# Kernel optimization log

Hardware: AMD Instinct MI355X
Metric: run time of the kernel (lower is better)

## Reference

```python
import jax, jax.numpy as jnp
import numpy as np

NUM_HEADS = 16


def setup_inputs() -> dict:
    key = jax.random.key(0)
    kq, kk, kv = jax.random.split(key, 3)
    b, s, h = 1, 4096, 1024
    q = jax.random.normal(kq, (b, s, h), dtype=jnp.float32)
    k = jax.random.normal(kk, (b, s, h), dtype=jnp.float32)
    v = jax.random.normal(kv, (b, s, h), dtype=jnp.float32)
    return {"q": q, "k": k, "v": v}


def reference(q, k, v):
    b, s, hd = q.shape
    n = NUM_HEADS
    d = hd // n
    # b s (n d) -> b s n d
    qh = q.reshape(b, s, n, d)
    kh = k.reshape(b, s, n, d)
    vh = v.reshape(b, s, n, d)
    scale = 1.0 / jnp.sqrt(jnp.float32(d))
    # non-causal flash-attention math: softmax(qk^T * scale) v
    scores = jnp.einsum('bqnd,bknd->bnqk', qh, kh) * scale  # [b, n, s, s]
    probs = jax.nn.softmax(scores, axis=-1)
    out = jnp.einsum('bnqk,bknd->bqnd', probs, vh)  # [b, s, n, d]
    return out.reshape(b, s, hd)
```

## Files before the change

kernel.cpp:

```cpp
#include <hip/hip_runtime.h>

#define S_   4096
#define H_   1024
#define NH_  16
#define NT_  64
#define SCALE_LOG2E 0.18033688011112042f

typedef __attribute__((ext_vector_type(8)))  short short8;
typedef __attribute__((ext_vector_type(16))) float f32x16;

__device__ __forceinline__ unsigned short f2bf(float x) {
    union { float f; unsigned u; } c; c.f = x;
    unsigned r = c.u + 0x7fffu + ((c.u >> 16) & 1u);
    return (unsigned short)(r >> 16);
}
__device__ __forceinline__ unsigned pk2(float a, float b) {
    return (unsigned)f2bf(a) | ((unsigned)f2bf(b) << 16);
}
__device__ __forceinline__ unsigned pkt(float a, float b) {
    union { float f; unsigned u; } ca, cb; ca.f = a; cb.f = b;
    return __builtin_amdgcn_perm(cb.u, ca.u, 0x07060302u);
}

__global__ __launch_bounds__(256) void prepack(
    const float* __restrict__ k, const float* __restrict__ v,
    unsigned short* __restrict__ kp, unsigned short* __restrict__ vtp)
{
    const int t  = threadIdx.x;
    const int kt = blockIdx.x, hd = blockIdx.y;
    const size_t tb = ((size_t)hd * NT_ + kt) * 4096;
    uint4* gk = (uint4*)(kp + tb);
    uint4* gv = (uint4*)(vtp + tb);

    #pragma unroll
    for (int it = 0; it < 2; ++it) {
        int idx = t + 256 * it;
        {
            int key = idx >> 3, kc = idx & 7;
            const float* src = k + (size_t)(kt * 64 + key) * H_ + hd * 64 + kc * 8;
            float4 a = *(const float4*)src;
            float4 b = *(const float4*)(src + 4);
            uint4 w;
            w.x = pk2(a.x, a.y); w.y = pk2(a.z, a.w);
            w.z = pk2(b.x, b.y); w.w = pk2(b.z, b.w);
            gk[kc * 64 + key] = w;
        }
        {
            int d = idx & 63, kc = idx >> 6;
            const float* src = v + (size_t)(kt * 64 + kc * 8) * H_ + hd * 64 + d;
            float p[8];
            #pragma unroll
            for (int j = 0; j < 8; ++j) p[j] = src[(size_t)j * H_];
            uint4 w;
            w.x = pk2(p[0], p[1]); w.y = pk2(p[2], p[3]);
            w.z = pk2(p[4], p[5]); w.w = pk2(p[6], p[7]);
            gv[idx] = w;
        }
    }
}

__global__ __launch_bounds__(256, 3) void attn_main(
    const float* __restrict__ q,
    const unsigned short* __restrict__ kp,
    const unsigned short* __restrict__ vtp,
    float* __restrict__ out)
{
    __shared__ __align__(16) float sO[2 * 2048];
    __shared__ float sL[2 * 64];

    const int t   = threadIdx.x;
    const int b   = blockIdx.x;
    const int xcd = b & 7;
    const int bi  = b >> 3;
    const int hd  = xcd * 2 + (bi >> 6);
    const int qt  = bi & 63;

    const int w    = t >> 6;
    const int lane = t & 63;
    const int l31  = lane & 31;
    const int lhi  = lane >> 5;
    const int qh   = w >> 1;
    const int kh   = w & 1;

    const unsigned short* gK = kp  + (size_t)hd * NT_ * 4096;
    const unsigned short* gV = vtp + (size_t)hd * NT_ * 4096;

    short8 qf[4];
    {
        const float* qb = q + (size_t)(qt * 64 + qh * 32 + l31) * H_ + hd * 64 + lhi * 8;
        #pragma unroll
        for (int c = 0; c < 4; ++c) {
            float4 a  = *(const float4*)(qb + c * 16);
            float4 bb = *(const float4*)(qb + c * 16 + 4);
            union { short8 v; unsigned u[4]; } f;
            f.u[0] = pk2(a.x * SCALE_LOG2E, a.y * SCALE_LOG2E);
            f.u[1] = pk2(a.z * SCALE_LOG2E, a.w * SCALE_LOG2E);
            f.u[2] = pk2(bb.x * SCALE_LOG2E, bb.y * SCALE_LOG2E);
            f.u[3] = pk2(bb.z * SCALE_LOG2E, bb.w * SCALE_LOG2E);
            qf[c] = f.v;
        }
    }

    f32x16 Oacc[2];
    #pragma unroll
    for (int h = 0; h < 2; ++h)
        #pragma unroll
        for (int r = 0; r < 16; ++r) Oacc[h][r] = 0.0f;
    float2 ls2; ls2.x = 0.0f; ls2.y = 0.0f;

    const int kOff = (kh * 32 + l31) * 8 + lhi * 512;
    const int vOff = l31 * 8 + (kh * 4 + lhi) * 512;
    const unsigned short* pK = gK + kOff;
    const unsigned short* pV = gV + vOff;

    short8 kfA[4], vfA[4], kfB[4], vfB[4];

#define LOADF(KF, VF, tile)                                                  \
    {                                                                        \
        const unsigned short* kt_ = pK + (size_t)(tile) * 4096;              \
        const unsigned short* vt_ = pV + (size_t)(tile) * 4096;              \
        KF[0] = *(const short8*)(kt_);                                       \
        KF[1] = *(const short8*)(kt_ + 1024);                                \
        KF[2] = *(const short8*)(kt_ + 2048);                                \
        KF[3] = *(const short8*)(kt_ + 3072);                                \
        VF[0] = *(const short8*)(vt_);                                       \
        VF[1] = *(const short8*)(vt_ + 256);                                 \
        VF[2] = *(const short8*)(vt_ + 1024);                                \
        VF[3] = *(const short8*)(vt_ + 1280);                                \
    }

#define COMPUTE(KF, VF)                                                      \
    {                                                                        \
        f32x16 st;                                                           \
        _Pragma("unroll")                                                    \
        for (int r_ = 0; r_ < 16; ++r_) st[r_] = 0.0f;                       \
        st = __builtin_amdgcn_mfma_f32_32x32x16_bf16(KF[0], qf[0], st, 0, 0, 0); \
        st = __builtin_amdgcn_mfma_f32_32x32x16_bf16(KF[1], qf[1], st, 0, 0, 0); \
        st = __builtin_amdgcn_mfma_f32_32x32x16_bf16(KF[2], qf[2], st, 0, 0, 0); \
        st = __builtin_amdgcn_mfma_f32_32x32x16_bf16(KF[3], qf[3], st, 0, 0, 0); \
        unsigned pu[8];                                                      \
        _Pragma("unroll")                                                    \
        for (int i2_ = 0; i2_ < 8; ++i2_) {                                  \
            float p0 = __builtin_amdgcn_exp2f(st[2 * i2_]);                  \
            float p1 = __builtin_amdgcn_exp2f(st[2 * i2_ + 1]);              \
            ls2.x += p0; ls2.y += p1;                                        \
            pu[i2_] = pkt(p0, p1);                                           \
        }                                                                    \
        _Pragma("unroll")                                                    \
        for (int c_ = 0; c_ < 2; ++c_) {                                     \
            unsigned a0 = pu[4 * c_],     b0 = pu[4 * c_ + 2];               \
            unsigned a1 = pu[4 * c_ + 1], b1 = pu[4 * c_ + 3];               \
                                   \
            asm("v_permlane32_swap_b32 %0, %1" : "+v"(a0), "+v"(b0));        \
            asm("v_permlane32_swap_b32 %0, %1" : "+v"(a1), "+v"(b1));        \
            union { short8 v; unsigned u[4]; } pf;                           \
            pf.u[0] = a0; pf.u[1] = a1; pf.u[2] = b0; pf.u[3] = b1;          \
            Oacc[0] = __builtin_amdgcn_mfma_f32_32x32x16_bf16(pf.v, VF[2 * c_],     Oacc[0], 0, 0, 0); \
            Oacc[1] = __builtin_amdgcn_mfma_f32_32x32x16_bf16(pf.v, VF[2 * c_ + 1], Oacc[1], 0, 0, 0); \
        }                                                                    \
    }

    LOADF(kfA, vfA, 0);
    for (int kt2 = 0; kt2 < 31; ++kt2) {
        LOADF(kfB, vfB, 2 * kt2 + 1);
        COMPUTE(kfA, vfA);
        LOADF(kfA, vfA, 2 * kt2 + 2);
        COMPUTE(kfB, vfB);
    }
    LOADF(kfB, vfB, 63);
    COMPUTE(kfA, vfA);
    COMPUTE(kfB, vfB);

#undef LOADF
#undef COMPUTE

    float lsum = ls2.x + ls2.y;
    lsum += __shfl_xor(lsum, 32);
    if (lhi == 0) sL[kh * 64 + qh * 32 + l31] = lsum;
    if (kh == 1) {
        float* o = sO + qh * 2048;
        #pragma unroll
        for (int h = 0; h < 2; ++h)
            #pragma unroll
            for (int r = 0; r < 16; ++r)
                o[h * 1024 + r * 64 + lane] = Oacc[h][r];
    }
    __syncthreads();
    if (kh == 0) {
        float linv[4][4];
        #pragma unroll
        for (int qd = 0; qd < 4; ++qd) {
            int base = qh * 32 + 8 * qd + 4 * lhi;
            float4 a  = *(const float4*)(sL + base);
            float4 bb = *(const float4*)(sL + 64 + base);
            linv[qd][0] = __builtin_amdgcn_rcpf(a.x + bb.x);
            linv[qd][1] = __builtin_amdgcn_rcpf(a.y + bb.y);
            linv[qd][2] = __builtin_amdgcn_rcpf(a.z + bb.z);
            linv[qd][3] = __builtin_amdgcn_rcpf(a.w + bb.w);
        }
        const float* o = sO + qh * 2048;
        #pragma unroll
        for (int h = 0; h < 2; ++h)
            #pragma unroll
            for (int qd = 0; qd < 4; ++qd)
                #pragma unroll
                for (int e = 0; e < 4; ++e) {
                    int r   = 4 * qd + e;
                    int row = qh * 32 + e + 8 * qd + 4 * lhi;
                    float val = (Oacc[h][r] + o[h * 1024 + r * 64 + lane]) * linv[qd][e];
                    out[(size_t)(qt * 64 + row) * H_ + hd * 64 + h * 32 + l31] = val;
                }
    }
}

extern "C" void kernel_launch(void* const* d_in, const int* in_sizes, int n_in,
                              void* d_out, int out_size, void* d_ws, size_t ws_size,
                              hipStream_t stream) {
    const float* q = (const float*)d_in[0];
    const float* k = (const float*)d_in[1];
    const float* v = (const float*)d_in[2];
    float* out = (float*)d_out;

    unsigned short* kp  = (unsigned short*)d_ws;
    unsigned short* vtp = kp + (size_t)NH_ * NT_ * 4096;

    prepack<<<dim3(NT_, NH_), 256, 0, stream>>>(k, v, kp, vtp);
    attn_main<<<dim3(1024), 256, 0, stream>>>(q, kp, vtp, out);
}
```

Before: 178.6 us.

## Double query tile per block to reuse K/V fragments across two query subtiles

Each warp now handles two 32-row query subtiles instead of one, so every K/V fragment loaded from global memory feeds twice as many MFMAs. The grid is halved to 512 blocks of 128 queries, and occupancy drops to 2 blocks per CU to make room for the larger accumulator register set. s_setprio hints are placed around the MFMA groups so this wave gets priority while the other waves run exp and permute work. The change cuts K/V load traffic per FLOP, at the cost of higher register pressure, fewer resident waves and only 512 blocks to spread across the CUs.

```diff
diff --git a/kernel.cpp b/kernel.cpp
--- a/kernel.cpp
+++ b/kernel.cpp
@@ -59,35 +59,36 @@
     }
 }
 
-__global__ __launch_bounds__(256, 3) void attn_main(
+__global__ __launch_bounds__(256, 2) void attn_main(
     const float* __restrict__ q,
     const unsigned short* __restrict__ kp,
     const unsigned short* __restrict__ vtp,
     float* __restrict__ out)
 {
-    __shared__ __align__(16) float sO[2 * 2048];
-    __shared__ float sL[2 * 64];
+    __shared__ __align__(16) float sO[4 * 2048];
+    __shared__ float sL[2 * 128];
 
     const int t   = threadIdx.x;
     const int b   = blockIdx.x;
     const int xcd = b & 7;
     const int bi  = b >> 3;
-    const int hd  = xcd * 2 + (bi >> 6);
-    const int qt  = bi & 63;
+    const int hd  = xcd * 2 + (bi >> 5);
+    const int qt  = bi & 31;
 
     const int w    = t >> 6;
     const int lane = t & 63;
     const int l31  = lane & 31;
     const int lhi  = lane >> 5;
-    const int qh   = w >> 1;
+    const int qg   = w >> 1;
     const int kh   = w & 1;
 
     const unsigned short* gK = kp  + (size_t)hd * NT_ * 4096;
     const unsigned short* gV = vtp + (size_t)hd * NT_ * 4096;
 
-    short8 qf[4];
-    {
-        const float* qb = q + (size_t)(qt * 64 + qh * 32 + l31) * H_ + hd * 64 + lhi * 8;
+    short8 qf[2][4];
+    #pragma unroll
+    for (int s = 0; s < 2; ++s) {
+        const float* qb = q + (size_t)(qt * 128 + qg * 64 + s * 32 + l31) * H_ + hd * 64 + lhi * 8;
         #pragma unroll
         for (int c = 0; c < 4; ++c) {
             float4 a  = *(const float4*)(qb + c * 16);
@@ -97,16 +98,23 @@
             f.u[1] = pk2(a.z * SCALE_LOG2E, a.w * SCALE_LOG2E);
             f.u[2] = pk2(bb.x * SCALE_LOG2E, bb.y * SCALE_LOG2E);
             f.u[3] = pk2(bb.z * SCALE_LOG2E, bb.w * SCALE_LOG2E);
-            qf[c] = f.v;
-        }
-    }
-
-    f32x16 Oacc[2];
-    #pragma unroll
-    for (int h = 0; h < 2; ++h)
-        #pragma unroll
-        for (int r = 0; r < 16; ++r) Oacc[h][r] = 0.0f;
-    float2 ls2; ls2.x = 0.0f; ls2.y = 0.0f;
+            qf[s][c] = f.v;
+        }
+    }
+
+    f32x16 Oacc[2][2];
+    #pragma unroll
+    for (int s = 0; s < 2; ++s)
+        #pragma unroll
+        for (int h = 0; h < 2; ++h)
+            #pragma unroll
+            for (int r = 0; r < 16; ++r) Oacc[s][h][r] = 0.0f;
+    float2 ls[2];
+    ls[0].x = 0.0f; ls[0].y = 0.0f; ls[1].x = 0.0f; ls[1].y = 0.0f;
+
+    f32x16 zero16;
+    #pragma unroll
+    for (int r = 0; r < 16; ++r) zero16[r] = 0.0f;
 
     const int kOff = (kh * 32 + l31) * 8 + lhi * 512;
     const int vOff = l31 * 8 + (kh * 4 + lhi) * 512;
@@ -131,32 +139,36 @@
 
 #define COMPUTE(KF, VF)                                                      \
     {                                                                        \
-        f32x16 st;                                                           \
         _Pragma("unroll")                                                    \
-        for (int r_ = 0; r_ < 16; ++r_) st[r_] = 0.0f;                       \
-        st = __builtin_amdgcn_mfma_f32_32x32x16_bf16(KF[0], qf[0], st, 0, 0, 0); \
-        st = __builtin_amdgcn_mfma_f32_32x32x16_bf16(KF[1], qf[1], st, 0, 0, 0); \
-        st = __builtin_amdgcn_mfma_f32_32x32x16_bf16(KF[2], qf[2], st, 0, 0, 0); \
-        st = __builtin_amdgcn_mfma_f32_32x32x16_bf16(KF[3], qf[3], st, 0, 0, 0); \
-        unsigned pu[8];                                                      \
-        _Pragma("unroll")                                                    \
-        for (int i2_ = 0; i2_ < 8; ++i2_) {                                  \
-            float p0 = __builtin_amdgcn_exp2f(st[2 * i2_]);                  \
-            float p1 = __builtin_amdgcn_exp2f(st[2 * i2_ + 1]);              \
-            ls2.x += p0; ls2.y += p1;                                        \
-            pu[i2_] = pkt(p0, p1);                                           \
-        }                                                                    \
-        _Pragma("unroll")                                                    \
-        for (int c_ = 0; c_ < 2; ++c_) {                                     \
-            unsigned a0 = pu[4 * c_],     b0 = pu[4 * c_ + 2];               \
-            unsigned a1 = pu[4 * c_ + 1], b1 = pu[4 * c_ + 3];               \
+        for (int s_ = 0; s_ < 2; ++s_) {                                     \
+            __builtin_amdgcn_s_setprio(1);                                   \
+            f32x16 st = __builtin_amdgcn_mfma_f32_32x32x16_bf16(KF[0], qf[s_][0], zero16, 0, 0, 0); \
+            st = __builtin_amdgcn_mfma_f32_32x32x16_bf16(KF[1], qf[s_][1], st, 0, 0, 0); \
+            st = __builtin_amdgcn_mfma_f32_32x32x16_bf16(KF[2], qf[s_][2], st, 0, 0, 0); \
+            st = __builtin_amdgcn_mfma_f32_32x32x16_bf16(KF[3], qf[s_][3], st, 0, 0, 0); \
+            __builtin_amdgcn_s_setprio(0);                                   \
+            unsigned pu[8];                                                  \
+            _Pragma("unroll")                                                \
+            for (int i2_ = 0; i2_ < 8; ++i2_) {                              \
+                float p0 = __builtin_amdgcn_exp2f(st[2 * i2_]);              \
+                float p1 = __builtin_amdgcn_exp2f(st[2 * i2_ + 1]);          \
+                ls[s_].x += p0; ls[s_].y += p1;                              \
+                pu[i2_] = pkt(p0, p1);                                       \
+            }                                                                \
+            _Pragma("unroll")                                                \
+            for (int c_ = 0; c_ < 2; ++c_) {                                 \
+                unsigned a0 = pu[4 * c_],     b0 = pu[4 * c_ + 2];           \
+                unsigned a1 = pu[4 * c_ + 1], b1 = pu[4 * c_ + 3];           \
                                    \
-            asm("v_permlane32_swap_b32 %0, %1" : "+v"(a0), "+v"(b0));        \
-            asm("v_permlane32_swap_b32 %0, %1" : "+v"(a1), "+v"(b1));        \
-            union { short8 v; unsigned u[4]; } pf;                           \
-            pf.u[0] = a0; pf.u[1] = a1; pf.u[2] = b0; pf.u[3] = b1;          \
-            Oacc[0] = __builtin_amdgcn_mfma_f32_32x32x16_bf16(pf.v, VF[2 * c_],     Oacc[0], 0, 0, 0); \
-            Oacc[1] = __builtin_amdgcn_mfma_f32_32x32x16_bf16(pf.v, VF[2 * c_ + 1], Oacc[1], 0, 0, 0); \
+                asm("v_permlane32_swap_b32 %0, %1" : "+v"(a0), "+v"(b0));    \
+                asm("v_permlane32_swap_b32 %0, %1" : "+v"(a1), "+v"(b1));    \
+                union { short8 v; unsigned u[4]; } pf;                       \
+                pf.u[0] = a0; pf.u[1] = a1; pf.u[2] = b0; pf.u[3] = b1;      \
+                __builtin_amdgcn_s_setprio(1);                               \
+                Oacc[s_][0] = __builtin_amdgcn_mfma_f32_32x32x16_bf16(pf.v, VF[2 * c_],     Oacc[s_][0], 0, 0, 0); \
+                Oacc[s_][1] = __builtin_amdgcn_mfma_f32_32x32x16_bf16(pf.v, VF[2 * c_ + 1], Oacc[s_][1], 0, 0, 0); \
+                __builtin_amdgcn_s_setprio(0);                               \
+            }                                                                \
         }                                                                    \
     }
 
@@ -174,42 +186,51 @@
 #undef LOADF
 #undef COMPUTE
 
-    float lsum = ls2.x + ls2.y;
-    lsum += __shfl_xor(lsum, 32);
-    if (lhi == 0) sL[kh * 64 + qh * 32 + l31] = lsum;
+    #pragma unroll
+    for (int s = 0; s < 2; ++s) {
+        float lsum = ls[s].x + ls[s].y;
+        lsum += __shfl_xor(lsum, 32);
+        if (lhi == 0) sL[kh * 128 + qg * 64 + s * 32 + l31] = lsum;
+    }
     if (kh == 1) {
-        float* o = sO + qh * 2048;
-        #pragma unroll
-        for (int h = 0; h < 2; ++h)
-            #pragma unroll
-            for (int r = 0; r < 16; ++r)
-                o[h * 1024 + r * 64 + lane] = Oacc[h][r];
+        #pragma unroll
+        for (int s = 0; s < 2; ++s) {
+            float* o = sO + (qg * 2 + s) * 2048;
+            #pragma unroll
+            for (int h = 0; h < 2; ++h)
+                #pragma unroll
+                for (int r = 0; r < 16; ++r)
+                    o[h * 1024 + r * 64 + lane] = Oacc[s][h][r];
+        }
     }
     __syncthreads();
     if (kh == 0) {
-        float linv[4][4];
-        #pragma unroll
-        for (int qd = 0; qd < 4; ++qd) {
-            int base = qh * 32 + 8 * qd + 4 * lhi;
-            float4 a  = *(const float4*)(sL + base);
-            float4 bb = *(const float4*)(sL + 64 + base);
-            linv[qd][0] = __builtin_amdgcn_rcpf(a.x + bb.x);
-            linv[qd][1] = __builtin_amdgcn_rcpf(a.y + bb.y);
-            linv[qd][2] = __builtin_amdgcn_rcpf(a.z + bb.z);
-            linv[qd][3] = __builtin_amdgcn_rcpf(a.w + bb.w);
-        }
-        const float* o = sO + qh * 2048;
-        #pragma unroll
-        for (int h = 0; h < 2; ++h)
-            #pragma unroll
-            for (int qd = 0; qd < 4; ++qd)
+        #pragma unroll
+        for (int s = 0; s < 2; ++s) {
+            float linv[4][4];
+            #pragma unroll
+            for (int qd = 0; qd < 4; ++qd) {
+                int base = qg * 64 + s * 32 + 8 * qd + 4 * lhi;
+                float4 a  = *(const float4*)(sL + base);
+                float4 bb = *(const float4*)(sL + 128 + base);
+                linv[qd][0] = __builtin_amdgcn_rcpf(a.x + bb.x);
+                linv[qd][1] = __builtin_amdgcn_rcpf(a.y + bb.y);
+                linv[qd][2] = __builtin_amdgcn_rcpf(a.z + bb.z);
+                linv[qd][3] = __builtin_amdgcn_rcpf(a.w + bb.w);
+            }
+            const float* o = sO + (qg * 2 + s) * 2048;
+            #pragma unroll
+            for (int h = 0; h < 2; ++h)
                 #pragma unroll
-                for (int e = 0; e < 4; ++e) {
-                    int r   = 4 * qd + e;
-                    int row = qh * 32 + e + 8 * qd + 4 * lhi;
-                    float val = (Oacc[h][r] + o[h * 1024 + r * 64 + lane]) * linv[qd][e];
-                    out[(size_t)(qt * 64 + row) * H_ + hd * 64 + h * 32 + l31] = val;
-                }
+                for (int qd = 0; qd < 4; ++qd)
+                    #pragma unroll
+                    for (int e = 0; e < 4; ++e) {
+                        int r   = 4 * qd + e;
+                        int row = e + 8 * qd + 4 * lhi;
+                        float val = (Oacc[s][h][r] + o[h * 1024 + r * 64 + lane]) * linv[qd][e];
+                        out[(size_t)(qt * 128 + qg * 64 + s * 32 + row) * H_ + hd * 64 + h * 32 + l31] = val;
+                    }
+        }
     }
 }
 
@@ -225,5 +246,5 @@
     unsigned short* vtp = kp + (size_t)NH_ * NT_ * 4096;
 
     prepack<<<dim3(NT_, NH_), 256, 0, stream>>>(k, v, kp, vtp);
-    attn_main<<<dim3(1024), 256, 0, stream>>>(q, kp, vtp, out);
-}
+    attn_main<<<dim3(512), 256, 0, stream>>>(q, kp, vtp, out);
+}
```

After: 164.7 us. -7.8%, faster.
